# Optimization experiments

Hardware: AMD Instinct MI355X
Metric: run time of the kernel (lower is better)

The kernel has to match this reference:

```python
import jax, jax.numpy as jnp
import numpy as np
from jax import lax

IMAGE_SIZE = 512
N_REWEIGHT = 3
BLUR_RADIUS = 4  # GaussianBlur(4)
BLUR_SIGMA = 4.0


def _cdist(a, b):
    # Euclidean distance matrix [N, M] via ||a||^2 + ||b||^2 - 2 a.b
    a2 = jnp.sum(a * a, axis=1)[:, None]
    b2 = jnp.sum(b * b, axis=1)[None, :]
    d2 = a2 + b2 - 2.0 * (a @ b.T)
    return jnp.sqrt(jnp.maximum(d2, 0.0))


def _gaussian_blur(img):
    # separable depthwise gaussian blur, kernel size 2*radius+1, SAME padding
    x = jnp.arange(-BLUR_RADIUS, BLUR_RADIUS + 1, dtype=img.dtype)
    g = jnp.exp(-(x * x) / (2.0 * BLUR_SIGMA * BLUR_SIGMA))
    g = g / jnp.sum(g)
    dn = ('NCHW', 'OIHW', 'NCHW')
    img = lax.conv_general_dilated(img, g.reshape(1, 1, -1, 1), (1, 1), 'SAME', dimension_numbers=dn)
    img = lax.conv_general_dilated(img, g.reshape(1, 1, 1, -1), (1, 1), 'SAME', dimension_numbers=dn)
    return img


def setup_inputs() -> dict:
    key = jax.random.key(0)
    k1, k2 = jax.random.split(key)
    h, w, d, m = 64, 64, 384, 65536
    patch = jax.random.normal(k1, (h * w, d), dtype=jnp.float32)
    patch_lib = jax.random.normal(k2, (m, d), dtype=jnp.float32)
    return {"patch": patch, "patch_lib": patch_lib, "fmap_h": h, "fmap_w": w}


def reference(patch, patch_lib, fmap_h, fmap_w):
    # dist: [N, M] full pairwise cdist against coreset library
    dist = _cdist(patch, patch_lib)
    min_val = jnp.min(dist, axis=1)            # [N] NN distance per test patch
    min_idx = jnp.argmin(dist, axis=1)         # [N]
    s_idx = jnp.argmax(min_val)
    s_star = jnp.max(min_val)
    m_test = patch[s_idx]                      # [D]
    m_star = patch_lib[min_idx[s_idx]]         # [D]
    # w_dist = cdist(m_star, patch_lib): single-row distance
    w_dist = jnp.sqrt(jnp.maximum(jnp.sum((m_star[None, :] - patch_lib) ** 2, axis=1), 0.0))
    neg_top, nn_idx = lax.top_k(-w_dist, N_REWEIGHT)   # k smallest
    m_star_knn = jnp.linalg.norm(m_test[None, :] - patch_lib[nn_idx[1:]], axis=1)  # [k-1]
    D = jnp.sqrt(jnp.asarray(patch.shape[1], dtype=patch.dtype))
    w = 1.0 - jnp.exp(s_star / D) / jnp.sum(jnp.exp(m_star_knn / D))
    s = w * s_star
    s_map = min_val.reshape(1, 1, fmap_h, fmap_w)
    s_map = jax.image.resize(s_map, (1, 1, IMAGE_SIZE, IMAGE_SIZE), method='bilinear')
    s_map = _gaussian_blur(s_map)
    return s, s_map
```

## Files before the change

### kernel.cpp

```cpp
#include <hip/hip_runtime.h>

#define NP 4096
#define DIM 384
#define ML 65536
#define INFF 3.402823466e38f

typedef int i32x4 __attribute__((ext_vector_type(4)));
typedef unsigned short u16;
typedef unsigned long long u64;

#define QSCALE 21.16666667f
#define INV2S2 0.0044640088f

typedef __attribute__((address_space(1))) unsigned int as1_u32;
typedef __attribute__((address_space(3))) unsigned int as3_u32;

__device__ __forceinline__ void gl_lds16(const void* g, void* l) {
  __builtin_amdgcn_global_load_lds((const as1_u32*)g, (as3_u32*)l, 16, 0, 0);
}

__global__ __launch_bounds__(256) void prep_kernel(const float* __restrict__ patch,
                                                   const float* __restrict__ lib,
                                                   char* __restrict__ Ai8,
                                                   char* __restrict__ Bi8,
                                                   float* __restrict__ a2,
                                                   float* __restrict__ b2) {
  const int row = blockIdx.x * 4 + (threadIdx.x >> 6);
  const int lane = threadIdx.x & 63;
  const float* src;
  char* dst;
  float* nrm;
  int r;
  if (row < NP) { src = patch; dst = Ai8; nrm = a2; r = row; }
  else          { src = lib;   dst = Bi8; nrm = b2; r = row - NP; }
  float s = 0.f;
#pragma unroll
  for (int j = 0; j < 3; ++j) {
    const float2 v = *reinterpret_cast<const float2*>(src + (size_t)r * DIM + j * 128 + lane * 2);
    s += v.x * v.x + v.y * v.y;
    const int q0 = __float2int_rn(fminf(fmaxf(v.x, -6.f), 6.f) * QSCALE);
    const int q1 = __float2int_rn(fminf(fmaxf(v.y, -6.f), 6.f) * QSCALE);
    const u16 p = (u16)((q0 & 0xFF) | ((q1 & 0xFF) << 8));
    *reinterpret_cast<u16*>(dst + (size_t)r * DIM + j * 128 + lane * 2) = p;
  }
#pragma unroll
  for (int m = 1; m < 64; m <<= 1) s += __shfl_xor(s, m);
  if (lane == 0) nrm[r] = s;
}

__global__ __launch_bounds__(512, 2) void gemm_min_kernel(const char* __restrict__ Ai8,
                                                          const char* __restrict__ Bi8,
                                                          const float* __restrict__ a2,
                                                          const float* __restrict__ b2,
                                                          u64* __restrict__ packed) {
  __shared__ __align__(16) char As[2][32768];
  __shared__ __align__(16) char Bs[2][32768];
  const int tid = threadIdx.x;
  const int lane = tid & 63;
  const int w = tid >> 6;
  const int wm = w >> 2;
  const int wn = w & 3;
  const int cl = lane & 15, rg = lane >> 4;

  const int orig = blockIdx.x;
  const int logical = (orig & 7) * 512 + (orig >> 3);
  const int xt = logical & 15;
  const int yt = logical >> 4;
  const int n0 = xt * 256;
  const int m0 = yt * 256;

  const char* ga[4]; const char* gb[4]; int lof[4];
#pragma unroll
  for (int i = 0; i < 4; ++i) {
    const int P = i * 8192 + tid * 16;
    const int r = P >> 7;
    const int L = P ^ ((r & 7) << 4);
    const int c = L & 127;
    lof[i] = P;
    ga[i] = Ai8 + (size_t)(n0 + r) * DIM + c;
    gb[i] = Bi8 + (size_t)(m0 + r) * DIM + c;
  }

  int offA[2][8], offB[2][4];
#pragma unroll
  for (int g = 0; g < 2; ++g) {
#pragma unroll
    for (int j = 0; j < 8; ++j) {
      const int row = wm * 128 + j * 16 + cl;
      offA[g][j] = row * 128 + ((g * 64 + rg * 16) ^ ((cl & 7) << 4));
    }
#pragma unroll
    for (int i = 0; i < 4; ++i) {
      const int row = wn * 64 + i * 16 + cl;
      offB[g][i] = row * 128 + ((g * 64 + rg * 16) ^ ((cl & 7) << 4));
    }
  }

  i32x4 acc[4][8] = {};

#pragma unroll
  for (int i = 0; i < 4; ++i) { gl_lds16(ga[i], (char*)As[0] + lof[i]); ga[i] += 128; }
#pragma unroll
  for (int i = 0; i < 4; ++i) { gl_lds16(gb[i], (char*)Bs[0] + lof[i]); gb[i] += 128; }

#pragma unroll
  for (int kt = 0; kt < 3; ++kt) {
    const int buf = kt & 1;
    if (kt < 2) {
#pragma unroll
      for (int i = 0; i < 4; ++i) { gl_lds16(ga[i], (char*)As[buf ^ 1] + lof[i]); ga[i] += 128; }
#pragma unroll
      for (int i = 0; i < 4; ++i) { gl_lds16(gb[i], (char*)Bs[buf ^ 1] + lof[i]); gb[i] += 128; }
      asm volatile("s_waitcnt vmcnt(8)" ::: "memory");
    } else {
      asm volatile("s_waitcnt vmcnt(0)" ::: "memory");
    }
    __builtin_amdgcn_s_barrier();
    __builtin_amdgcn_sched_barrier(0);

    const char* Ab = (const char*)As[buf];
    const char* Bb = (const char*)Bs[buf];
#pragma unroll
    for (int g = 0; g < 2; ++g) {
      i32x4 af[8], bg[4];
#pragma unroll
      for (int j = 0; j < 8; ++j)
        af[j] = *reinterpret_cast<const i32x4*>(Ab + offA[g][j]);
#pragma unroll
      for (int i = 0; i < 4; ++i)
        bg[i] = *reinterpret_cast<const i32x4*>(Bb + offB[g][i]);
#pragma unroll
      for (int i = 0; i < 4; ++i)
#pragma unroll
        for (int j = 0; j < 8; ++j)
          acc[i][j] = __builtin_amdgcn_mfma_i32_16x16x64_i8(bg[i], af[j], acc[i][j], 0, 0, 0);
    }
    __builtin_amdgcn_s_barrier();
    __builtin_amdgcn_sched_barrier(0);
  }

  const int colb = m0 + wn * 64 + rg * 4;
  float bc[4][4];
#pragma unroll
  for (int i = 0; i < 4; ++i)
#pragma unroll
    for (int r = 0; r < 4; ++r) bc[i][r] = b2[colb + i * 16 + r];

  u64* sh = reinterpret_cast<u64*>(As);

#pragma unroll
  for (int j = 0; j < 8; ++j) {
    const int prow = wm * 128 + j * 16 + cl;
    const float ar = a2[n0 + prow];
    u64 best = ~0ull;
#pragma unroll
    for (int i = 0; i < 4; ++i)
#pragma unroll
      for (int r = 0; r < 4; ++r) {
        const float d2 = fmaxf(ar + bc[i][r] - INV2S2 * (float)acc[i][j][r], 0.0f);
        const u64 p = ((u64)__float_as_uint(d2) << 32) | (unsigned)(colb + i * 16 + r);
        best = p < best ? p : best;
      }
    const u64 o1 = __shfl_xor(best, 16); best = o1 < best ? o1 : best;
    const u64 o2 = __shfl_xor(best, 32); best = o2 < best ? o2 : best;
    if (rg == 0) sh[prow * 4 + wn] = best;
  }
  __syncthreads();
  if (tid < 256) {
    u64 v = sh[tid * 4];
#pragma unroll
    for (int k = 1; k < 4; ++k) { const u64 o = sh[tid * 4 + k]; v = o < v ? o : v; }
    atomicMin(&packed[n0 + tid], v);
  }
}

__global__ __launch_bounds__(256) void exactmin_kernel(const float* __restrict__ patch,
                                                       const float* __restrict__ lib,
                                                       u64* __restrict__ packed) {
  const int n = blockIdx.x * 4 + (threadIdx.x >> 6);
  const int lane = threadIdx.x & 63;
  const int idx = (int)(unsigned)packed[n];
  float s = 0.f;
#pragma unroll
  for (int j = 0; j < 3; ++j) {
    const float2 a = *reinterpret_cast<const float2*>(patch + (size_t)n * DIM + j * 128 + lane * 2);
    const float2 b = *reinterpret_cast<const float2*>(lib + (size_t)idx * DIM + j * 128 + lane * 2);
    const float d0 = a.x - b.x, d1 = a.y - b.y;
    s += d0 * d0 + d1 * d1;
  }
#pragma unroll
  for (int m = 1; m < 64; m <<= 1) s += __shfl_xor(s, m);
  if (lane == 0) packed[n] = ((u64)__float_as_uint(fmaxf(s, 0.f)) << 32) | (unsigned)idx;
}

__global__ __launch_bounds__(256) void cand_kernel(const u64* __restrict__ packed,
                                                   int* __restrict__ cand) {
  const int tid = threadIdx.x;
  float mx = -1.f;
  for (int n = tid; n < NP; n += 256) {
    const float v = __uint_as_float((unsigned)(packed[n] >> 32));
    mx = fmaxf(mx, v);
  }
#pragma unroll
  for (int m = 1; m < 64; m <<= 1) mx = fmaxf(mx, __shfl_xor(mx, m));
  __shared__ float wmax[4];
  __shared__ float smax;
  if ((tid & 63) == 0) wmax[tid >> 6] = mx;
  __syncthreads();
  if (tid == 0) {
    smax = fmaxf(fmaxf(wmax[0], wmax[1]), fmaxf(wmax[2], wmax[3]));
    cand[0] = 0;
  }
  __syncthreads();
  const float thr = smax - 6.0f;
  for (int n = tid; n < NP; n += 256) {
    const float v = __uint_as_float((unsigned)(packed[n] >> 32));
    if (v >= thr) {
      const int slot = atomicAdd(&cand[0], 1);
      if (slot < 256) cand[1 + slot] = n;
    }
  }
}

__global__ __launch_bounds__(256) void refine_kernel(const float* __restrict__ patch,
                                                     const float* __restrict__ lib,
                                                     const int* __restrict__ cand,
                                                     u64* __restrict__ refined) {
  const int cnt = min(cand[0], 256);
  const int tid = threadIdx.x, lane = tid & 63, w = tid >> 6;
  const int base = blockIdx.x * 32;
  __shared__ float a[8][DIM];
  __shared__ u64 rb[8][4];

  for (int g0 = 0; g0 < cnt; g0 += 8) {
    const int gc = min(cnt - g0, 8);
    for (int i = tid; i < gc * DIM; i += 256) {
      const int c = i / DIM, e = i - c * DIM;
      a[c][e] = patch[(size_t)cand[1 + g0 + c] * DIM + e];
    }
    __syncthreads();

    u64 wbest[8];
#pragma unroll
    for (int c = 0; c < 8; ++c) wbest[c] = ~0ull;

    for (int it = 0; it < 8; ++it) {
      const int m = base + w * 8 + it;
      float lr[6];
#pragma unroll
      for (int j = 0; j < 3; ++j) {
        const float2 v = *reinterpret_cast<const float2*>(lib + (size_t)m * DIM + j * 128 + lane * 2);
        lr[j * 2] = v.x; lr[j * 2 + 1] = v.y;
      }
#pragma unroll
      for (int c = 0; c < 8; ++c) {
        if (c >= gc) break;
        float s = 0.f;
#pragma unroll
        for (int j = 0; j < 3; ++j) {
          const float d0 = lr[j * 2] - a[c][j * 128 + lane * 2];
          const float d1 = lr[j * 2 + 1] - a[c][j * 128 + lane * 2 + 1];
          s += d0 * d0 + d1 * d1;
        }
#pragma unroll
        for (int msk = 1; msk < 64; msk <<= 1) s += __shfl_xor(s, msk);
        const u64 p = ((u64)__float_as_uint(s) << 32) | (unsigned)m;
        wbest[c] = p < wbest[c] ? p : wbest[c];
      }
    }
    if (lane == 0) {
#pragma unroll
      for (int c = 0; c < 8; ++c)
        if (c < gc) rb[c][w] = wbest[c];
    }
    __syncthreads();
    if (tid < gc) {
      u64 b = rb[tid][0];
#pragma unroll
      for (int k = 1; k < 4; ++k) b = rb[tid][k] < b ? rb[tid][k] : b;
      atomicMin(&refined[g0 + tid], b);
    }
    __syncthreads();
  }
}

__global__ __launch_bounds__(256) void pick_kernel(const u64* __restrict__ refined,
                                                   const int* __restrict__ cand,
                                                   int* __restrict__ scal_i,
                                                   float* __restrict__ scal_f) {
  const int tid = threadIdx.x, lane = tid & 63, w = tid >> 6;
  const int cnt = min(cand[0], 256);
  float v = -1.f;
  int nrow = 0x7FFFFFFF;
  int mi = 0;
  if (tid < cnt) {
    const u64 p = refined[tid];
    v = __uint_as_float((unsigned)(p >> 32));
    nrow = cand[1 + tid];
    mi = (int)(unsigned)p;
  }
#pragma unroll
  for (int msk = 1; msk < 64; msk <<= 1) {
    const float ov = __shfl_xor(v, msk);
    const int on = __shfl_xor(nrow, msk);
    const int om = __shfl_xor(mi, msk);
    if (ov > v || (ov == v && on < nrow)) { v = ov; nrow = on; mi = om; }
  }
  __shared__ float sv[4]; __shared__ int sn[4]; __shared__ int sm[4];
  if (lane == 0) { sv[w] = v; sn[w] = nrow; sm[w] = mi; }
  __syncthreads();
  if (tid == 0) {
    for (int k = 1; k < 4; ++k)
      if (sv[k] > v || (sv[k] == v && sn[k] < nrow)) { v = sv[k]; nrow = sn[k]; mi = sm[k]; }
    scal_i[0] = nrow;
    scal_i[1] = mi;
    scal_f[0] = sqrtf(fmaxf(v, 0.f));
  }
}

__device__ __forceinline__ void ins3u(u64 x, u64* v) {
  if (x < v[2]) {
    v[2] = x;
    if (v[2] < v[1]) { u64 t = v[1]; v[1] = v[2]; v[2] = t; }
    if (v[1] < v[0]) { u64 t = v[0]; v[0] = v[1]; v[1] = t; }
  }
}

__global__ __launch_bounds__(256) void wtop_kernel(const float* __restrict__ lib,
                                                   const int* __restrict__ scal_i,
                                                   u64* __restrict__ t3) {
  __shared__ float a[DIM];
  __shared__ u64 sv[12];
  const int tid = threadIdx.x, lane = tid & 63, w = tid >> 6;
  const int ms = scal_i[1];
  for (int i = tid; i < DIM; i += 256) a[i] = lib[(size_t)ms * DIM + i];
  __syncthreads();
  const int base = blockIdx.x * 32;
  u64 v[3] = {~0ull, ~0ull, ~0ull};
  for (int it = 0; it < 8; ++it) {
    const int m = base + w * 8 + it;
    float s = 0.f;
#pragma unroll
    for (int j = 0; j < 3; ++j) {
      const float2 lv = *reinterpret_cast<const float2*>(lib + (size_t)m * DIM + j * 128 + lane * 2);
      const float d0 = lv.x - a[j * 128 + lane * 2];
      const float d1 = lv.y - a[j * 128 + lane * 2 + 1];
      s += d0 * d0 + d1 * d1;
    }
#pragma unroll
    for (int msk = 1; msk < 64; msk <<= 1) s += __shfl_xor(s, msk);
    ins3u(((u64)__float_as_uint(s) << 32) | (unsigned)m, v);
  }
  if (lane == 0) {
#pragma unroll
    for (int k = 0; k < 3; ++k) sv[w * 3 + k] = v[k];
  }
  __syncthreads();
  if (tid == 0) {
    u64 fv[3] = {~0ull, ~0ull, ~0ull};
    for (int k = 0; k < 12; ++k) ins3u(sv[k], fv);
#pragma unroll
    for (int k = 0; k < 3; ++k) t3[blockIdx.x * 3 + k] = fv[k];
  }
}

__global__ __launch_bounds__(256) void final_kernel(const u64* __restrict__ t3,
                                                    const float* __restrict__ patch,
                                                    const float* __restrict__ lib,
                                                    const int* __restrict__ scal_i,
                                                    const float* __restrict__ scal_f,
                                                    float* __restrict__ out) {
  const int tid = threadIdx.x, lane = tid & 63, w = tid >> 6;
  u64 v[3] = {~0ull, ~0ull, ~0ull};
  for (int i = tid; i < 6144; i += 256) ins3u(t3[i], v);
#pragma unroll
  for (int msk = 1; msk < 64; msk <<= 1) {
    u64 o0 = __shfl_xor(v[0], msk);
    u64 o1 = __shfl_xor(v[1], msk);
    u64 o2 = __shfl_xor(v[2], msk);
    ins3u(o0, v); ins3u(o1, v); ins3u(o2, v);
  }
  __shared__ u64 sv[12];
  __shared__ int nn[2]; __shared__ float kk[2];
  if (lane == 0) {
#pragma unroll
    for (int k = 0; k < 3; ++k) sv[w * 3 + k] = v[k];
  }
  __syncthreads();
  if (tid == 0) {
    u64 fv[3] = {~0ull, ~0ull, ~0ull};
    for (int k = 0; k < 12; ++k) ins3u(sv[k], fv);
    nn[0] = (int)(unsigned)fv[1];
    nn[1] = (int)(unsigned)fv[2];
  }
  __syncthreads();
  if (w < 2) {
    const int s_idx = scal_i[0];
    const int nnx = nn[w];
    float s = 0.f;
#pragma unroll
    for (int k = 0; k < 6; ++k) {
      const float d = patch[(size_t)s_idx * DIM + lane + k * 64] - lib[(size_t)nnx * DIM + lane + k * 64];
      s += d * d;
    }
#pragma unroll
    for (int msk = 1; msk < 64; msk <<= 1) s += __shfl_xor(s, msk);
    if (lane == 0) kk[w] = sqrtf(s);
  }
  __syncthreads();
  if (tid == 0) {
    const float s_star = scal_f[0];
    const float Ds = 19.59591794f;
    const float wt = 1.0f - expf(s_star / Ds) / (expf(kk[0] / Ds) + expf(kk[1] / Ds));
    out[0] = wt * s_star;
  }
}

__device__ __constant__ float BW[9] = {
    0.0816741424f, 0.1016453893f, 0.1188358540f, 0.1305155396f, 0.1346581512f,
    0.1305155396f, 0.1188358540f, 0.1016453893f, 0.0816741424f};

__global__ __launch_bounds__(256) void scoremap_kernel(const u64* __restrict__ packed,
                                                       float* __restrict__ out) {
  __shared__ float mv[4096];
  __shared__ float t1b[12][512];
  __shared__ float t2b[4][512];
  const int tid = threadIdx.x;
  const int y0 = blockIdx.x * 4;

  for (int i = tid; i < 4096; i += 256)
    mv[i] = sqrtf(fmaxf(__uint_as_float((unsigned)(packed[i] >> 32)), 0.f));
  __syncthreads();

  for (int i = tid; i < 12 * 512; i += 256) {
    const int ry = i >> 9, x = i & 511;
    const int y = y0 - 4 + ry;
    float v = 0.f;
    if (y >= 0 && y < 512) {
      const float sy = y * 0.125f - 0.4375f;
      const float sx = x * 0.125f - 0.4375f;
      const int yy = (int)floorf(sy); const float fy = sy - (float)yy;
      const int xx = (int)floorf(sx); const float fx = sx - (float)xx;
      const int ya = max(yy, 0), yb = min(yy + 1, 63);
      const int xa = max(xx, 0), xb = min(xx + 1, 63);
      v = (1.f - fy) * ((1.f - fx) * mv[ya * 64 + xa] + fx * mv[ya * 64 + xb]) +
          fy * ((1.f - fx) * mv[yb * 64 + xa] + fx * mv[yb * 64 + xb]);
    }
    t1b[ry][x] = v;
  }
  __syncthreads();

  for (int i = tid; i < 4 * 512; i += 256) {
    const int r = i >> 9, x = i & 511;
    float s = 0.f;
#pragma unroll
    for (int k = -4; k <= 4; ++k) s += BW[k + 4] * t1b[r + 4 + k][x];
    t2b[r][x] = s;
  }
  __syncthreads();

  for (int i = tid; i < 4 * 512; i += 256) {
    const int r = i >> 9, x = i & 511;
    float s = 0.f;
#pragma unroll
    for (int k = -4; k <= 4; ++k) {
      const int xx = x + k;
      if (xx >= 0 && xx < 512) s += BW[k + 4] * t2b[r][xx];
    }
    out[(y0 + r) * 512 + x] = s;
  }
}

extern "C" void kernel_launch(void* const* d_in, const int* in_sizes, int n_in,
                              void* d_out, int out_size, void* d_ws, size_t ws_size,
                              hipStream_t stream) {
  const float* patch = (const float*)d_in[0];
  const float* lib = (const float*)d_in[1];
  float* out = (float*)d_out;

  char* ws = (char*)d_ws;
  size_t off = 0;
  auto alloc = [&](size_t bytes) {
    void* p = ws + off;
    off += (bytes + 255) & ~(size_t)255;
    return p;
  };
  char* Ai8 = (char*)alloc((size_t)NP * DIM);
  char* Bi8 = (char*)alloc((size_t)ML * DIM);
  float* a2 = (float*)alloc(NP * 4);
  float* b2 = (float*)alloc(ML * 4);
  u64* packed = (u64*)alloc(NP * 8);
  u64* refined = (u64*)alloc(256 * 8);
  int* cand = (int*)alloc(257 * 4);
  int* scal_i = (int*)alloc(64);
  float* scal_f = (float*)alloc(64);
  u64* t3 = (u64*)alloc(2048 * 3 * 8);

  hipMemsetAsync(packed, 0xFF, NP * 8, stream);
  hipMemsetAsync(refined, 0xFF, 256 * 8, stream);

  prep_kernel<<<(NP + ML) / 4, 256, 0, stream>>>(patch, lib, Ai8, Bi8, a2, b2);
  gemm_min_kernel<<<4096, 512, 0, stream>>>(Ai8, Bi8, a2, b2, packed);
  exactmin_kernel<<<NP / 4, 256, 0, stream>>>(patch, lib, packed);
  cand_kernel<<<1, 256, 0, stream>>>(packed, cand);
  refine_kernel<<<2048, 256, 0, stream>>>(patch, lib, cand, refined);
  pick_kernel<<<1, 256, 0, stream>>>(refined, cand, scal_i, scal_f);
  wtop_kernel<<<2048, 256, 0, stream>>>(lib, scal_i, t3);
  final_kernel<<<1, 256, 0, stream>>>(t3, patch, lib, scal_i, scal_f, out);
  scoremap_kernel<<<128, 256, 0, stream>>>(packed, out + 1);
}
```

Baseline: 269.1 us.

## Load int8 GEMM fragments directly from global and use integer distance keys

```diff
diff --git a/kernel.cpp b/kernel.cpp
--- a/kernel.cpp
+++ b/kernel.cpp
@@ -3,36 +3,27 @@
 #define NP 4096
 #define DIM 384
 #define ML 65536
-#define INFF 3.402823466e38f
 
 typedef int i32x4 __attribute__((ext_vector_type(4)));
 typedef unsigned short u16;
 typedef unsigned long long u64;
 
 #define QSCALE 21.16666667f
-#define INV2S2 0.0044640088f
-
-typedef __attribute__((address_space(1))) unsigned int as1_u32;
-typedef __attribute__((address_space(3))) unsigned int as3_u32;
-
-__device__ __forceinline__ void gl_lds16(const void* g, void* l) {
-  __builtin_amdgcn_global_load_lds((const as1_u32*)g, (as3_u32*)l, 16, 0, 0);
-}
+#define B2SCALE 224.0138889f
+#define KBIAS (1 << 23)
 
 __global__ __launch_bounds__(256) void prep_kernel(const float* __restrict__ patch,
                                                    const float* __restrict__ lib,
                                                    char* __restrict__ Ai8,
                                                    char* __restrict__ Bi8,
-                                                   float* __restrict__ a2,
-                                                   float* __restrict__ b2) {
+                                                   int* __restrict__ b2i) {
   const int row = blockIdx.x * 4 + (threadIdx.x >> 6);
   const int lane = threadIdx.x & 63;
   const float* src;
   char* dst;
-  float* nrm;
   int r;
-  if (row < NP) { src = patch; dst = Ai8; nrm = a2; r = row; }
-  else          { src = lib;   dst = Bi8; nrm = b2; r = row - NP; }
+  if (row < NP) { src = patch; dst = Ai8; r = row; }
+  else          { src = lib;   dst = Bi8; r = row - NP; }
   float s = 0.f;
 #pragma unroll
   for (int j = 0; j < 3; ++j) {
@@ -45,16 +36,14 @@
   }
 #pragma unroll
   for (int m = 1; m < 64; m <<= 1) s += __shfl_xor(s, m);
-  if (lane == 0) nrm[r] = s;
+  if (lane == 0 && row >= NP) b2i[r] = __float2int_rn(s * B2SCALE);
 }
 
 __global__ __launch_bounds__(512, 2) void gemm_min_kernel(const char* __restrict__ Ai8,
                                                           const char* __restrict__ Bi8,
-                                                          const float* __restrict__ a2,
-                                                          const float* __restrict__ b2,
+                                                          const int* __restrict__ b2i,
                                                           u64* __restrict__ packed) {
-  __shared__ __align__(16) char As[2][32768];
-  __shared__ __align__(16) char Bs[2][32768];
+  __shared__ u64 sh[1024];
   const int tid = threadIdx.x;
   const int lane = tid & 63;
   const int w = tid >> 6;
@@ -69,96 +58,49 @@
   const int n0 = xt * 256;
   const int m0 = yt * 256;
 
-  const char* ga[4]; const char* gb[4]; int lof[4];
-#pragma unroll
-  for (int i = 0; i < 4; ++i) {
-    const int P = i * 8192 + tid * 16;
-    const int r = P >> 7;
-    const int L = P ^ ((r & 7) << 4);
-    const int c = L & 127;
-    lof[i] = P;
-    ga[i] = Ai8 + (size_t)(n0 + r) * DIM + c;
-    gb[i] = Bi8 + (size_t)(m0 + r) * DIM + c;
-  }
-
-  int offA[2][8], offB[2][4];
-#pragma unroll
-  for (int g = 0; g < 2; ++g) {
-#pragma unroll
-    for (int j = 0; j < 8; ++j) {
-      const int row = wm * 128 + j * 16 + cl;
-      offA[g][j] = row * 128 + ((g * 64 + rg * 16) ^ ((cl & 7) << 4));
-    }
-#pragma unroll
-    for (int i = 0; i < 4; ++i) {
-      const int row = wn * 64 + i * 16 + cl;
-      offB[g][i] = row * 128 + ((g * 64 + rg * 16) ^ ((cl & 7) << 4));
-    }
-  }
+  const char* ar[8];
+#pragma unroll
+  for (int j = 0; j < 8; ++j)
+    ar[j] = Ai8 + (size_t)(n0 + wm * 128 + j * 16 + cl) * DIM + rg * 16;
+  const char* br[4];
+#pragma unroll
+  for (int i = 0; i < 4; ++i)
+    br[i] = Bi8 + (size_t)(m0 + wn * 64 + i * 16 + cl) * DIM + rg * 16;
 
   i32x4 acc[4][8] = {};
 
 #pragma unroll
-  for (int i = 0; i < 4; ++i) { gl_lds16(ga[i], (char*)As[0] + lof[i]); ga[i] += 128; }
-#pragma unroll
-  for (int i = 0; i < 4; ++i) { gl_lds16(gb[i], (char*)Bs[0] + lof[i]); gb[i] += 128; }
-
-#pragma unroll
-  for (int kt = 0; kt < 3; ++kt) {
-    const int buf = kt & 1;
-    if (kt < 2) {
-#pragma unroll
-      for (int i = 0; i < 4; ++i) { gl_lds16(ga[i], (char*)As[buf ^ 1] + lof[i]); ga[i] += 128; }
-#pragma unroll
-      for (int i = 0; i < 4; ++i) { gl_lds16(gb[i], (char*)Bs[buf ^ 1] + lof[i]); gb[i] += 128; }
-      asm volatile("s_waitcnt vmcnt(8)" ::: "memory");
-    } else {
-      asm volatile("s_waitcnt vmcnt(0)" ::: "memory");
-    }
-    __builtin_amdgcn_s_barrier();
-    __builtin_amdgcn_sched_barrier(0);
-
-    const char* Ab = (const char*)As[buf];
-    const char* Bb = (const char*)Bs[buf];
-#pragma unroll
-    for (int g = 0; g < 2; ++g) {
-      i32x4 af[8], bg[4];
+  for (int s = 0; s < 6; ++s) {
+    i32x4 af[8], bg[4];
+#pragma unroll
+    for (int j = 0; j < 8; ++j)
+      af[j] = *reinterpret_cast<const i32x4*>(ar[j] + s * 64);
+#pragma unroll
+    for (int i = 0; i < 4; ++i)
+      bg[i] = *reinterpret_cast<const i32x4*>(br[i] + s * 64);
+#pragma unroll
+    for (int i = 0; i < 4; ++i)
 #pragma unroll
       for (int j = 0; j < 8; ++j)
-        af[j] = *reinterpret_cast<const i32x4*>(Ab + offA[g][j]);
-#pragma unroll
-      for (int i = 0; i < 4; ++i)
-        bg[i] = *reinterpret_cast<const i32x4*>(Bb + offB[g][i]);
-#pragma unroll
-      for (int i = 0; i < 4; ++i)
-#pragma unroll
-        for (int j = 0; j < 8; ++j)
-          acc[i][j] = __builtin_amdgcn_mfma_i32_16x16x64_i8(bg[i], af[j], acc[i][j], 0, 0, 0);
-    }
-    __builtin_amdgcn_s_barrier();
-    __builtin_amdgcn_sched_barrier(0);
+        acc[i][j] = __builtin_amdgcn_mfma_i32_16x16x64_i8(bg[i], af[j], acc[i][j], 0, 0, 0);
   }
 
   const int colb = m0 + wn * 64 + rg * 4;
-  float bc[4][4];
+  i32x4 bc[4];
 #pragma unroll
   for (int i = 0; i < 4; ++i)
-#pragma unroll
-    for (int r = 0; r < 4; ++r) bc[i][r] = b2[colb + i * 16 + r];
-
-  u64* sh = reinterpret_cast<u64*>(As);
+    bc[i] = *reinterpret_cast<const i32x4*>(&b2i[colb + i * 16]);
 
 #pragma unroll
   for (int j = 0; j < 8; ++j) {
     const int prow = wm * 128 + j * 16 + cl;
-    const float ar = a2[n0 + prow];
     u64 best = ~0ull;
 #pragma unroll
     for (int i = 0; i < 4; ++i)
 #pragma unroll
       for (int r = 0; r < 4; ++r) {
-        const float d2 = fmaxf(ar + bc[i][r] - INV2S2 * (float)acc[i][j][r], 0.0f);
-        const u64 p = ((u64)__float_as_uint(d2) << 32) | (unsigned)(colb + i * 16 + r);
+        const unsigned kb = (unsigned)(bc[i][r] - acc[i][j][r] + KBIAS);
+        const u64 p = ((u64)kb << 32) | (unsigned)(colb + i * 16 + r);
         best = p < best ? p : best;
       }
     const u64 o1 = __shfl_xor(best, 16); best = o1 < best ? o1 : best;
@@ -212,7 +154,7 @@
     cand[0] = 0;
   }
   __syncthreads();
-  const float thr = smax - 6.0f;
+  const float thr = smax - 8.0f;
   for (int n = tid; n < NP; n += 256) {
     const float v = __uint_as_float((unsigned)(packed[n] >> 32));
     if (v >= thr) {
@@ -487,8 +429,7 @@
   };
   char* Ai8 = (char*)alloc((size_t)NP * DIM);
   char* Bi8 = (char*)alloc((size_t)ML * DIM);
-  float* a2 = (float*)alloc(NP * 4);
-  float* b2 = (float*)alloc(ML * 4);
+  int* b2i = (int*)alloc(ML * 4);
   u64* packed = (u64*)alloc(NP * 8);
   u64* refined = (u64*)alloc(256 * 8);
   int* cand = (int*)alloc(257 * 4);
@@ -499,8 +440,8 @@
   hipMemsetAsync(packed, 0xFF, NP * 8, stream);
   hipMemsetAsync(refined, 0xFF, 256 * 8, stream);
 
-  prep_kernel<<<(NP + ML) / 4, 256, 0, stream>>>(patch, lib, Ai8, Bi8, a2, b2);
-  gemm_min_kernel<<<4096, 512, 0, stream>>>(Ai8, Bi8, a2, b2, packed);
+  prep_kernel<<<(NP + ML) / 4, 256, 0, stream>>>(patch, lib, Ai8, Bi8, b2i);
+  gemm_min_kernel<<<4096, 512, 0, stream>>>(Ai8, Bi8, b2i, packed);
   exactmin_kernel<<<NP / 4, 256, 0, stream>>>(patch, lib, packed);
   cand_kernel<<<1, 256, 0, stream>>>(packed, cand);
   refine_kernel<<<2048, 256, 0, stream>>>(patch, lib, cand, refined);
```

New measurement: 435.8 us. 62.0% more time.
